# Kernel tuning notes

Measured on AMD Instinct MI355X. Metric: run time of the kernel, lower is better.

## Reference

```python
import jax, jax.numpy as jnp
import numpy as np

BLOCK_SIZE = 3
SOBEL_PAD = 1  # sobel_size // 2
BLOCK_PAD = BLOCK_SIZE // 2

_SOBEL_X = jnp.array([[-1.0, 0.0, 1.0], [-2.0, 0.0, 2.0], [-1.0, 0.0, 1.0]], dtype=jnp.float32)[None, None]
_SOBEL_Y = jnp.array([[-1.0, -2.0, -1.0], [0.0, 0.0, 0.0], [1.0, 2.0, 1.0]], dtype=jnp.float32)[None, None]
_SUM_K = jnp.ones((1, 1, BLOCK_SIZE, BLOCK_SIZE), dtype=jnp.float32)


def _pad_replicate(x, p):
    return jnp.pad(x, ((0, 0), (0, 0), (p, p), (p, p)), mode='edge')


def _conv(x, k):
    return jax.lax.conv_general_dilated(
        x, k, window_strides=(1, 1), padding='VALID',
        dimension_numbers=('NCHW', 'OIHW', 'NCHW'))


def setup_inputs() -> dict:
    key = jax.random.key(0)
    image = jax.random.uniform(key, (8, 1, 1080, 1920), dtype=jnp.float32) * 255.0
    return {"image": image}


def reference(image) -> jnp.ndarray:
    img = image.astype(jnp.float32)
    img_p = _pad_replicate(img, SOBEL_PAD)
    Ix = _conv(img_p, _SOBEL_X)
    Iy = _conv(img_p, _SOBEL_Y)
    Ixx = Ix * Ix
    Iyy = Iy * Iy
    Ixy = Ix * Iy
    sum_Ixx = _conv(_pad_replicate(Ixx, BLOCK_PAD), _SUM_K)
    sum_Iyy = _conv(_pad_replicate(Iyy, BLOCK_PAD), _SUM_K)
    sum_Ixy = _conv(_pad_replicate(Ixy, BLOCK_PAD), _SUM_K)
    half_trace = (sum_Ixx + sum_Iyy) * 0.5
    diff_half = (sum_Ixx - sum_Iyy) * 0.5
    sqrt_disc = jnp.sqrt(diff_half * diff_half + sum_Ixy * sum_Ixy + 1e-10)
    lambda_min = half_trace - sqrt_disc
    return jnp.clip(lambda_min, 0.0)
```

## Files before the change

### kernel.cpp

```cpp
#include <hip/hip_runtime.h>

typedef float v4f __attribute__((ext_vector_type(4)));

#define IMG_H 1080
#define IMG_W 1920
#define NBATCH 8
#define LSTRIP 9
#define BROWS (4*LSTRIP)
#define NK (LSTRIP+4)
#define PF 3
#define RS 4


__global__ __launch_bounds__(256, 2)
void shi_tomasi_kernel(const float* __restrict__ img, float* __restrict__ out) {
    const int cg    = threadIdx.x & 63;
    const int strip = threadIdx.x >> 6;
    const int bx    = blockIdx.x;
    const int base  = bx * 240;
    const int c0    = base + 4 * (cg - 2);
    const int clA   = min(max(c0 - 2, 0), IMG_W - 4);
    const int clB   = min(max(c0 + 2, 0), IMG_W - 4);
    const int s0    = blockIdx.y * BROWS + strip * LSTRIP;
    const float* g  = img + (size_t)blockIdx.z * (IMG_H * IMG_W);
    float* outb     = out + (size_t)blockIdx.z * (IMG_H * IMG_W);

    const bool eL     = (bx == 0) && (cg == 2);
    const bool eR     = (bx == 7) && (cg == 61);
    const bool doSt   = (cg >= 2) && (cg < 62);
    const bool topFix = (s0 == 0);
    const bool botFix = (s0 + LSTRIP == IMG_H);

    const float* lpA = g + clA;
    const float* lpB = g + clB;

    v4f za[RS], zb[RS];
    #pragma unroll
    for (int k = 0; k < PF; ++k) {
        int lr = max(0, min(IMG_H - 1, s0 - 2 + k));
        za[k] = *(const v4f*)(lpA + (size_t)lr * IMG_W);
        zb[k] = *(const v4f*)(lpB + (size_t)lr * IMG_W);
    }

    float cdR[3][6], hsR[3][6];
    float hxx[3][4], hyy[3][4], hxy[3][4];

    #pragma unroll
    for (int k = 0; k < NK; ++k) {
        if (k + PF < NK) {
            int lr = min(IMG_H - 1, s0 + k + (PF - 2));
            za[(k + PF) % RS] = *(const v4f*)(lpA + (size_t)lr * IMG_W);
            zb[(k + PF) % RS] = *(const v4f*)(lpB + (size_t)lr * IMG_W);
        }

        {
            const v4f A = za[k % RS];
            const v4f B = zb[k % RS];
            const float zm2 = A.x;
            const float zm1 = eL ? A.x : A.y;
            const float z0  = eL ? A.x : A.z;
            const float z1  = eL ? A.y : A.w;
            const float z2  = eR ? B.z : B.x;
            const float z3  = eR ? B.w : B.y;
            const float z4  = eR ? B.w : B.z;
            const float z5  = B.w;

            float* cdw = cdR[k % 3];
            float* hsw = hsR[k % 3];
            cdw[0] = z0 - zm2;
            cdw[1] = z1 - zm1;
            cdw[2] = z2 - z0;
            cdw[3] = z3 - z1;
            cdw[4] = z4 - z2;
            cdw[5] = z5 - z3;
            hsw[0] = fmaf(2.0f, zm1, zm2) + z0;
            hsw[1] = fmaf(2.0f, z0, zm1) + z1;
            hsw[2] = fmaf(2.0f, z1, z0) + z2;
            hsw[3] = fmaf(2.0f, z2, z1) + z3;
            hsw[4] = fmaf(2.0f, z3, z2) + z4;
            hsw[5] = fmaf(2.0f, z4, z3) + z5;
        }

        if (k >= 2) {
            const int rr = k - 2;
            const int sm = rr % 3, sz = (rr + 1) % 3, sp = (rr + 2) % 3;

            float Ix[6], Iy[6];
            #pragma unroll
            for (int p = 0; p < 6; ++p) {
                Ix[p] = fmaf(2.0f, cdR[sz][p], cdR[sm][p]) + cdR[sp][p];
                Iy[p] = hsR[sp][p] - hsR[sm][p];
            }
            if (eL) { Ix[0] = Ix[1]; Iy[0] = Iy[1]; }
            if (eR) { Ix[5] = Ix[4]; Iy[5] = Iy[4]; }

            float xx[6], yy[6], xy[6];
            #pragma unroll
            for (int p = 0; p < 6; ++p) {
                xx[p] = Ix[p] * Ix[p];
                yy[p] = Iy[p] * Iy[p];
                xy[p] = Ix[p] * Iy[p];
            }
            {
                float* hx = hxx[rr % 3];
                float* hy = hyy[rr % 3];
                float* hz = hxy[rr % 3];
                #pragma unroll
                for (int c = 0; c < 4; ++c) {
                    hx[c] = (xx[c] + xx[c + 1]) + xx[c + 2];
                    hy[c] = (yy[c] + yy[c + 1]) + yy[c + 2];
                    hz[c] = (xy[c] + xy[c + 1]) + xy[c + 2];
                }
            }
            if (rr == 1 && topFix) {
                #pragma unroll
                for (int c = 0; c < 4; ++c) {
                    hxx[0][c] = hxx[1][c]; hyy[0][c] = hyy[1][c]; hxy[0][c] = hxy[1][c];
                }
            }
            if (rr == LSTRIP + 1 && botFix) {
                #pragma unroll
                for (int c = 0; c < 4; ++c) {
                    hxx[rr % 3][c] = hxx[(rr - 1) % 3][c];
                    hyy[rr % 3][c] = hyy[(rr - 1) % 3][c];
                    hxy[rr % 3][c] = hxy[(rr - 1) % 3][c];
                }
            }

            if (rr >= 2) {
                const int a = (rr - 2) % 3, b2 = (rr - 1) % 3, cc = rr % 3;
                float rv[4];
                #pragma unroll
                for (int c = 0; c < 4; ++c) {
                    const float sxx = (hxx[a][c] + hxx[b2][c]) + hxx[cc][c];
                    const float syy = (hyy[a][c] + hyy[b2][c]) + hyy[cc][c];
                    const float sxy = (hxy[a][c] + hxy[b2][c]) + hxy[cc][c];
                    const float S = sxx + syy;
                    const float D = sxx - syy;
                    const float E = sxy + sxy;
                    const float disc = fmaf(D, D, fmaf(E, E, 4e-10f));
                    const float q = __builtin_sqrtf(disc);
                    rv[c] = fmaxf((S - q) * 0.5f, 0.0f);
                }
                if (doSt) {
                    float* orowp = outb + (size_t)(s0 + rr - 2) * IMG_W + c0;
                    __builtin_nontemporal_store(v4f{rv[0], rv[1], rv[2], rv[3]},
                                                (v4f*)orowp);
                }
            }
        }
    }
}

extern "C" void kernel_launch(void* const* d_in, const int* in_sizes, int n_in,
                              void* d_out, int out_size, void* d_ws, size_t ws_size,
                              hipStream_t stream) {
    const float* img = (const float*)d_in[0];
    float* out = (float*)d_out;
    dim3 grid(8, IMG_H / BROWS, NBATCH);
    shi_tomasi_kernel<<<grid, 256, 0, stream>>>(img, out);
}
```

Baseline: 117.3 us.

## Widen per-thread tile to 8 output columns and halve grid width

Each thread now computes 8 output columns instead of 4. It loads four aligned float4 vectors per row, and the grid has half as many blocks in x. This amortises the 2-column halo on each side over more outputs, cutting redundant loads and recomputed Sobel/box sums per output, and it issues two vector stores per row. The prefetch depth is reduced from 3 rows to 2 to limit register growth, so latency hiding may get worse and the number of resident blocks shrinks.

After: 127.1 us. 1.08x slower.

```diff
diff --git a/kernel.cpp b/kernel.cpp
--- a/kernel.cpp
+++ b/kernel.cpp
@@ -8,8 +8,9 @@
 #define LSTRIP 9
 #define BROWS (4*LSTRIP)
 #define NK (LSTRIP+4)
-#define PF 3
-#define RS 4
+#define PF 2
+#define RS 2
+#define PXL 8
 
 
 __global__ __launch_bounds__(256, 2)
@@ -17,86 +18,88 @@
     const int cg    = threadIdx.x & 63;
     const int strip = threadIdx.x >> 6;
     const int bx    = blockIdx.x;
-    const int base  = bx * 240;
-    const int c0    = base + 4 * (cg - 2);
-    const int clA   = min(max(c0 - 2, 0), IMG_W - 4);
-    const int clB   = min(max(c0 + 2, 0), IMG_W - 4);
+    const int c0    = bx * 480 + PXL * (cg - 2);
+    const int clA   = min(max(c0 - 4, 0), IMG_W - 4);
+    const int clB   = min(max(c0,     0), IMG_W - 4);
+    const int clC   = min(max(c0 + 4, 0), IMG_W - 4);
+    const int clD   = min(max(c0 + 8, 0), IMG_W - 4);
     const int s0    = blockIdx.y * BROWS + strip * LSTRIP;
     const float* g  = img + (size_t)blockIdx.z * (IMG_H * IMG_W);
     float* outb     = out + (size_t)blockIdx.z * (IMG_H * IMG_W);
 
     const bool eL     = (bx == 0) && (cg == 2);
-    const bool eR     = (bx == 7) && (cg == 61);
+    const bool eR     = (bx == 3) && (cg == 61);
     const bool doSt   = (cg >= 2) && (cg < 62);
     const bool topFix = (s0 == 0);
     const bool botFix = (s0 + LSTRIP == IMG_H);
 
     const float* lpA = g + clA;
     const float* lpB = g + clB;
+    const float* lpC = g + clC;
+    const float* lpD = g + clD;
 
-    v4f za[RS], zb[RS];
+    v4f zA[RS], zB[RS], zC[RS], zD[RS];
     #pragma unroll
     for (int k = 0; k < PF; ++k) {
-        int lr = max(0, min(IMG_H - 1, s0 - 2 + k));
-        za[k] = *(const v4f*)(lpA + (size_t)lr * IMG_W);
-        zb[k] = *(const v4f*)(lpB + (size_t)lr * IMG_W);
+        const size_t ro = (size_t)max(0, s0 - 2 + k) * IMG_W;
+        zA[k % RS] = *(const v4f*)(lpA + ro);
+        zB[k % RS] = *(const v4f*)(lpB + ro);
+        zC[k % RS] = *(const v4f*)(lpC + ro);
+        zD[k % RS] = *(const v4f*)(lpD + ro);
     }
 
-    float cdR[3][6], hsR[3][6];
-    float hxx[3][4], hyy[3][4], hxy[3][4];
+    float cdR[3][10], hsR[3][10];
+    float hxx[3][8], hyy[3][8], hxy[3][8];
 
     #pragma unroll
     for (int k = 0; k < NK; ++k) {
+        const v4f A = zA[k % RS];
+        const v4f B = zB[k % RS];
+        const v4f C = zC[k % RS];
+        const v4f D = zD[k % RS];
+
         if (k + PF < NK) {
-            int lr = min(IMG_H - 1, s0 + k + (PF - 2));
-            za[(k + PF) % RS] = *(const v4f*)(lpA + (size_t)lr * IMG_W);
-            zb[(k + PF) % RS] = *(const v4f*)(lpB + (size_t)lr * IMG_W);
+            const size_t ro = (size_t)min(IMG_H - 1, s0 + k) * IMG_W;
+            zA[k % RS] = *(const v4f*)(lpA + ro);
+            zB[k % RS] = *(const v4f*)(lpB + ro);
+            zC[k % RS] = *(const v4f*)(lpC + ro);
+            zD[k % RS] = *(const v4f*)(lpD + ro);
         }
 
         {
-            const v4f A = za[k % RS];
-            const v4f B = zb[k % RS];
-            const float zm2 = A.x;
-            const float zm1 = eL ? A.x : A.y;
-            const float z0  = eL ? A.x : A.z;
-            const float z1  = eL ? A.y : A.w;
-            const float z2  = eR ? B.z : B.x;
-            const float z3  = eR ? B.w : B.y;
-            const float z4  = eR ? B.w : B.z;
-            const float z5  = B.w;
+            float zw[12];
+            zw[0]  = eL ? B.x : A.z;
+            zw[1]  = eL ? B.x : A.w;
+            zw[2]  = B.x; zw[3] = B.y; zw[4] = B.z; zw[5] = B.w;
+            zw[6]  = C.x; zw[7] = C.y; zw[8] = C.z; zw[9] = C.w;
+            zw[10] = eR ? C.w : D.x;
+            zw[11] = eR ? C.w : D.y;
 
             float* cdw = cdR[k % 3];
             float* hsw = hsR[k % 3];
-            cdw[0] = z0 - zm2;
-            cdw[1] = z1 - zm1;
-            cdw[2] = z2 - z0;
-            cdw[3] = z3 - z1;
-            cdw[4] = z4 - z2;
-            cdw[5] = z5 - z3;
-            hsw[0] = fmaf(2.0f, zm1, zm2) + z0;
-            hsw[1] = fmaf(2.0f, z0, zm1) + z1;
-            hsw[2] = fmaf(2.0f, z1, z0) + z2;
-            hsw[3] = fmaf(2.0f, z2, z1) + z3;
-            hsw[4] = fmaf(2.0f, z3, z2) + z4;
-            hsw[5] = fmaf(2.0f, z4, z3) + z5;
+            #pragma unroll
+            for (int i = 0; i < 10; ++i) {
+                cdw[i] = zw[i + 2] - zw[i];
+                hsw[i] = fmaf(2.0f, zw[i + 1], zw[i]) + zw[i + 2];
+            }
         }
 
         if (k >= 2) {
             const int rr = k - 2;
             const int sm = rr % 3, sz = (rr + 1) % 3, sp = (rr + 2) % 3;
 
-            float Ix[6], Iy[6];
+            float Ix[10], Iy[10];
             #pragma unroll
-            for (int p = 0; p < 6; ++p) {
+            for (int p = 0; p < 10; ++p) {
                 Ix[p] = fmaf(2.0f, cdR[sz][p], cdR[sm][p]) + cdR[sp][p];
                 Iy[p] = hsR[sp][p] - hsR[sm][p];
             }
             if (eL) { Ix[0] = Ix[1]; Iy[0] = Iy[1]; }
-            if (eR) { Ix[5] = Ix[4]; Iy[5] = Iy[4]; }
+            if (eR) { Ix[9] = Ix[8]; Iy[9] = Iy[8]; }
 
-            float xx[6], yy[6], xy[6];
+            float xx[10], yy[10], xy[10];
             #pragma unroll
-            for (int p = 0; p < 6; ++p) {
+            for (int p = 0; p < 10; ++p) {
                 xx[p] = Ix[p] * Ix[p];
                 yy[p] = Iy[p] * Iy[p];
                 xy[p] = Ix[p] * Iy[p];
@@ -106,7 +109,7 @@
                 float* hy = hyy[rr % 3];
                 float* hz = hxy[rr % 3];
                 #pragma unroll
-                for (int c = 0; c < 4; ++c) {
+                for (int c = 0; c < 8; ++c) {
                     hx[c] = (xx[c] + xx[c + 1]) + xx[c + 2];
                     hy[c] = (yy[c] + yy[c + 1]) + yy[c + 2];
                     hz[c] = (xy[c] + xy[c + 1]) + xy[c + 2];
@@ -114,13 +117,13 @@
             }
             if (rr == 1 && topFix) {
                 #pragma unroll
-                for (int c = 0; c < 4; ++c) {
+                for (int c = 0; c < 8; ++c) {
                     hxx[0][c] = hxx[1][c]; hyy[0][c] = hyy[1][c]; hxy[0][c] = hxy[1][c];
                 }
             }
             if (rr == LSTRIP + 1 && botFix) {
                 #pragma unroll
-                for (int c = 0; c < 4; ++c) {
+                for (int c = 0; c < 8; ++c) {
                     hxx[rr % 3][c] = hxx[(rr - 1) % 3][c];
                     hyy[rr % 3][c] = hyy[(rr - 1) % 3][c];
                     hxy[rr % 3][c] = hxy[(rr - 1) % 3][c];
@@ -129,16 +132,16 @@
 
             if (rr >= 2) {
                 const int a = (rr - 2) % 3, b2 = (rr - 1) % 3, cc = rr % 3;
-                float rv[4];
+                float rv[8];
                 #pragma unroll
-                for (int c = 0; c < 4; ++c) {
+                for (int c = 0; c < 8; ++c) {
                     const float sxx = (hxx[a][c] + hxx[b2][c]) + hxx[cc][c];
                     const float syy = (hyy[a][c] + hyy[b2][c]) + hyy[cc][c];
                     const float sxy = (hxy[a][c] + hxy[b2][c]) + hxy[cc][c];
                     const float S = sxx + syy;
-                    const float D = sxx - syy;
+                    const float Dd = sxx - syy;
                     const float E = sxy + sxy;
-                    const float disc = fmaf(D, D, fmaf(E, E, 4e-10f));
+                    const float disc = fmaf(Dd, Dd, fmaf(E, E, 4e-10f));
                     const float q = __builtin_sqrtf(disc);
                     rv[c] = fmaxf((S - q) * 0.5f, 0.0f);
                 }
@@ -146,6 +149,8 @@
                     float* orowp = outb + (size_t)(s0 + rr - 2) * IMG_W + c0;
                     __builtin_nontemporal_store(v4f{rv[0], rv[1], rv[2], rv[3]},
                                                 (v4f*)orowp);
+                    __builtin_nontemporal_store(v4f{rv[4], rv[5], rv[6], rv[7]},
+                                                (v4f*)(orowp + 4));
                 }
             }
         }
@@ -157,6 +162,6 @@
                               hipStream_t stream) {
     const float* img = (const float*)d_in[0];
     float* out = (float*)d_out;
-    dim3 grid(8, IMG_H / BROWS, NBATCH);
+    dim3 grid(4, IMG_H / BROWS, NBATCH);
     shi_tomasi_kernel<<<grid, 256, 0, stream>>>(img, out);
 }
```
